# Optimization experiments

Hardware: AMD Instinct MI355X
Metric: run time of the kernel (lower is better)

The kernel has to match this reference:

```python
import jax, jax.numpy as jnp
import numpy as np

N, D, NUM_CLASSES = 4096, 1024, 1000


def setup_inputs() -> dict:
    key = jax.random.key(0)
    k1, k2 = jax.random.split(key)
    output = jax.random.normal(k1, (N, D), dtype=jnp.float32)
    target = jax.random.randint(k2, (N,), 0, NUM_CLASSES, dtype=jnp.int64)
    return {"output": output, "target": target}


def reference(output, target):
    # k1: strictly-lower-triangular part of the gram matrix [N, N]
    gram = output @ output.T
    k1 = jnp.tril(gram, -1)
    # k2: strictly-lower-triangular label-equality mask (vectorized form of
    # the original O(N^2) python double loop)
    eq = (target[:, None] == target[None, :]).astype(output.dtype)
    k2 = jnp.tril(eq, -1)
    return -(jnp.sum(k1 * k2) / (jnp.sum(k2) * jnp.linalg.norm(k1)))
```

## Files before the change

### kernel.cpp

```cpp
#include <hip/hip_runtime.h>
#include <hip/hip_bf16.h>


typedef __attribute__((ext_vector_type(8))) short short8;
typedef __attribute__((ext_vector_type(4))) float f32x4;

#define N_ROWS 4096
#define D_DIM  1024
#define N_CLS  1000
#define NTILE  32
#define NBLK   528
#define NK     32

__device__ __forceinline__ unsigned short f2bf(float f) {
  unsigned u = __float_as_uint(f);
  u += 0x7fffu + ((u >> 16) & 1u);
  return (unsigned short)(u >> 16);
}

__device__ __forceinline__ void gload16(const short* g, const char* l) {
  __builtin_amdgcn_global_load_lds(
      (const __attribute__((address_space(1))) unsigned*)g,
      (__attribute__((address_space(3))) unsigned*)(void*)l, 16, 0, 0);
}

__global__ void __launch_bounds__(256) kprep(const float* __restrict__ A,
                                             const int* __restrict__ target,
                                             short* __restrict__ Ab,
                                             double* __restrict__ rowp,
                                             double* __restrict__ cssp,
                                             int* __restrict__ cntp) {
  const int tid = threadIdx.x, lane = tid & 63, w = tid >> 6;

  if (blockIdx.x < 512) {
    __shared__ double wr2[4];
    const int row0 = blockIdx.x * 8;
    double ls = 0.0;
#pragma unroll
    for (int rr = 0; rr < 2; ++rr) {
      const int i = row0 + w * 2 + rr;
      const float4* src = (const float4*)(A + (size_t)i * D_DIM);
      short4* dst = (short4*)(Ab + (size_t)i * D_DIM);
      float s = 0.f;
#pragma unroll
      for (int c = 0; c < 4; ++c) {
        const float4 v = src[lane + c * 64];
        s += v.x * v.x + v.y * v.y + v.z * v.z + v.w * v.w;
        short4 o;
        o.x = (short)f2bf(v.x); o.y = (short)f2bf(v.y);
        o.z = (short)f2bf(v.z); o.w = (short)f2bf(v.w);
        dst[lane + c * 64] = o;
      }
#pragma unroll
      for (int off = 32; off; off >>= 1) s += __shfl_down(s, off);
      if (lane == 0) ls += (double)s;
    }
    if (lane == 0) wr2[w] = ls;
    __syncthreads();
    if (tid == 0) rowp[blockIdx.x] = wr2[0] + wr2[1] + wr2[2] + wr2[3];
  } else {
    __shared__ int list[N_ROWS];
    __shared__ int lcnt;
    __shared__ float wred[4];
    const int c = blockIdx.x - 512;
    if (c >= N_CLS) return;
    if (tid == 0) lcnt = 0;
    __syncthreads();
    for (int j = tid; j < N_ROWS; j += 256)
      if (target[j] == c) { int p = atomicAdd(&lcnt, 1); list[p] = j; }
    __syncthreads();
    const int n = lcnt;
    float4 acc = make_float4(0.f, 0.f, 0.f, 0.f);
    for (int m = 0; m < n; ++m) {
      const float4 v = *(const float4*)(A + (size_t)list[m] * D_DIM + tid * 4);
      acc.x += v.x; acc.y += v.y; acc.z += v.z; acc.w += v.w;
    }
    float s = acc.x * acc.x + acc.y * acc.y + acc.z * acc.z + acc.w * acc.w;
#pragma unroll
    for (int off = 32; off; off >>= 1) s += __shfl_down(s, off);
    if (lane == 0) wred[w] = s;
    __syncthreads();
    if (tid == 0) {
      cssp[c] = (double)(wred[0] + wred[1] + wred[2] + wred[3]);
      cntp[c] = n;
    }
  }
}

__global__ void __launch_bounds__(256, 2) kfrob(const short* __restrict__ Ab,
                                                double* __restrict__ frobp) {
  __shared__ __align__(16) short As[2][128 * 32];
  __shared__ __align__(16) short Bs[2][128 * 32];
  __shared__ double wred[4];
  const int tid = threadIdx.x, lane = tid & 63, w = tid >> 6;

  const int b = (blockIdx.x & 7) * 66 + (blockIdx.x >> 3);

  int bi = (int)((sqrtf(8.f * (float)b + 1.f) - 1.f) * 0.5f);
  while ((bi + 1) * (bi + 2) / 2 <= b) ++bi;
  while (bi * (bi + 1) / 2 > b) --bi;
  const int bj = b - bi * (bi + 1) / 2;
  const bool diag = (bi == bj);

  const short* Pa = Ab + (size_t)(bi * 128) * D_DIM;
  const short* Pb = Ab + (size_t)(bj * 128) * D_DIM;

  f32x4 acc[4][4];
#pragma unroll
  for (int m = 0; m < 4; ++m)
#pragma unroll
    for (int n = 0; n < 4; ++n) acc[m][n] = (f32x4){0.f, 0.f, 0.f, 0.f};

  const int wr = w >> 1, wc = w & 1;
  const int row16 = lane & 15, ck = lane >> 4;

  const int sr = tid >> 2;
  const int scS = (tid & 3) ^ ((sr >> 1) & 3);
  const size_t g0 = (size_t)sr * D_DIM + scS * 8;
  const size_t g1 = (size_t)(sr + 64) * D_DIM + scS * 8;
  const int l0 = w * 1024;
  const int l1 = 4096 + w * 1024;

#define STAGE(buf, k0)                                                      \
  do {                                                                      \
    gload16(Pa + g0 + (k0), (const char*)As[buf] + l0);                     \
    gload16(Pa + g1 + (k0), (const char*)As[buf] + l1);                     \
    gload16(Pb + g0 + (k0), (const char*)Bs[buf] + l0);                     \
    gload16(Pb + g1 + (k0), (const char*)Bs[buf] + l1);                     \
  } while (0)

#define SWZ(R) (((R) * 32) + ((ck ^ (((R) >> 1) & 3)) * 8))

#define COMPUTE(buf)                                                        \
  do {                                                                      \
    short8 af[4], bf[4];                                                    \
    _Pragma("unroll")                                                       \
    for (int m = 0; m < 4; ++m)                                             \
      af[m] = *(const short8*)&As[buf][SWZ(wr * 64 + m * 16 + row16)];      \
    _Pragma("unroll")                                                       \
    for (int n = 0; n < 4; ++n)                                             \
      bf[n] = *(const short8*)&Bs[buf][SWZ(wc * 64 + n * 16 + row16)];      \
    _Pragma("unroll")                                                       \
    for (int m = 0; m < 4; ++m)                                             \
      _Pragma("unroll")                                                     \
      for (int n = 0; n < 4; ++n)                                           \
        acc[m][n] = __builtin_amdgcn_mfma_f32_16x16x32_bf16(af[m], bf[n],   \
                                                            acc[m][n], 0, 0, 0);\
  } while (0)

  STAGE(0, 0);
  int cur = 0;
#pragma unroll 1
  for (int t = 0; t < NK - 1; ++t) {
    STAGE(cur ^ 1, (t + 1) * 32);
    asm volatile("s_waitcnt vmcnt(4)" ::: "memory");
    __builtin_amdgcn_sched_barrier(0);
    __builtin_amdgcn_s_barrier();
    __builtin_amdgcn_sched_barrier(0);
    COMPUTE(cur);
    asm volatile("s_waitcnt lgkmcnt(0)" ::: "memory");
    __builtin_amdgcn_sched_barrier(0);
    __builtin_amdgcn_s_barrier();
    __builtin_amdgcn_sched_barrier(0);
    cur ^= 1;
  }
  asm volatile("s_waitcnt vmcnt(0)" ::: "memory");
  __builtin_amdgcn_sched_barrier(0);
  __builtin_amdgcn_s_barrier();
  __builtin_amdgcn_sched_barrier(0);
  COMPUTE(cur);
#undef STAGE
#undef COMPUTE
#undef SWZ

  float fs = 0.f;
  if (!diag) {
#pragma unroll
    for (int m = 0; m < 4; ++m)
#pragma unroll
      for (int n = 0; n < 4; ++n)
#pragma unroll
        for (int q = 0; q < 4; ++q) fs += acc[m][n][q] * acc[m][n][q];
  } else {
    const int rbase = (lane >> 4) * 4, cbase = lane & 15;
#pragma unroll
    for (int m = 0; m < 4; ++m)
#pragma unroll
      for (int n = 0; n < 4; ++n)
#pragma unroll
        for (int q = 0; q < 4; ++q) {
          const int rl = wr * 64 + m * 16 + rbase + q;
          const int cl = wc * 64 + n * 16 + cbase;
          if (rl > cl) fs += acc[m][n][q] * acc[m][n][q];
        }
  }
#pragma unroll
  for (int off = 32; off; off >>= 1) fs += __shfl_down(fs, off);
  if (lane == 0) wred[w] = (double)fs;
  __syncthreads();
  if (tid == 0)
    frobp[b] = wred[0] + wred[1] + wred[2] + wred[3];
}

__global__ void __launch_bounds__(256) kfinal(const double* __restrict__ rowp,
                                              const double* __restrict__ cssp,
                                              const int* __restrict__ cntp,
                                              const double* __restrict__ frobp,
                                              float* __restrict__ out) {
  __shared__ double red[256];
  const int tid = threadIdx.x;
  double lsum = rowp[tid] + rowp[tid + 256];
  double lcss = 0.0, lcnn = 0.0, lfr = 0.0;
  for (int c = tid; c < N_CLS; c += 256) {
    lcss += cssp[c];
    const double nc = (double)cntp[c];
    lcnn += nc * nc;
  }
  for (int c = tid; c < NBLK; c += 256) lfr += frobp[c];

  double vals[4] = {lsum, lcss, lcnn, lfr};
  double res[4];
  for (int v = 0; v < 4; ++v) {
    red[tid] = vals[v];
    __syncthreads();
    for (int s = 128; s; s >>= 1) {
      if (tid < s) red[tid] += red[tid + s];
      __syncthreads();
    }
    res[v] = red[0];
    __syncthreads();
  }
  if (tid == 0) {
    const double sumr = res[0], css = res[1], cnn = res[2], frob = res[3];
    const double S1 = 0.5 * (css - sumr);
    const double S2 = 0.5 * (cnn - (double)N_ROWS);
    const double S3 = frob;
    out[0] = (float)(-(S1 / (S2 * sqrt(S3))));
  }
}

extern "C" void kernel_launch(void* const* d_in, const int* in_sizes, int n_in,
                              void* d_out, int out_size, void* d_ws, size_t ws_size,
                              hipStream_t stream) {
  const float* A = (const float*)d_in[0];
  const int* target = (const int*)d_in[1];
  float* out = (float*)d_out;

  char* ws = (char*)d_ws;
  short*  Ab    = (short*)ws;
  double* rowp  = (double*)(ws + 8388608);
  double* cssp  = (double*)(ws + 8388608 + 4096);
  int*    cntp  = (int*)   (ws + 8388608 + 4096 + 8000);
  double* frobp = (double*)(ws + 8388608 + 4096 + 8000 + 4096);

  kprep<<<512 + N_CLS, 256, 0, stream>>>(A, target, Ab, rowp, cssp, cntp);
  kfrob<<<NBLK, 256, 0, stream>>>(Ab, frobp);
  kfinal<<<1, 256, 0, stream>>>(rowp, cssp, cntp, frobp, out);
}
```

Before: 46.96 us.

## Compute Frobenius norm via small D×D Gram matrix A^T A with split-K

Uses the identity ||AA^T||_F^2 = ||A^T A||_F^2, so the Gram is computed on the 1024x1024 A^T A (symmetric lower tiles) instead of the 4096x4096 output. The prep kernel now transposes A to bf16 and stores per-row squared norms; the strict-lower sum is recovered as half of (total minus the sum of squared row norms). The GEMM is split across 8 K-chunks writing partial tiles to a slab, with a new reduction kernel summing them. This cuts matmul work roughly fourfold but adds a transpose, a large slab write/read and an extra launch. Subtracting the diagonal term may also cost precision.

```diff
diff --git a/kernel.cpp b/kernel.cpp
--- a/kernel.cpp
+++ b/kernel.cpp
@@ -8,9 +8,9 @@
 #define N_ROWS 4096
 #define D_DIM  1024
 #define N_CLS  1000
-#define NTILE  32
-#define NBLK   528
-#define NK     32
+#define NCHUNK 8
+#define NTIL   36
+#define NKG    16
 
 __device__ __forceinline__ unsigned short f2bf(float f) {
   unsigned u = __float_as_uint(f);
@@ -26,43 +26,46 @@
 
 __global__ void __launch_bounds__(256) kprep(const float* __restrict__ A,
                                              const int* __restrict__ target,
-                                             short* __restrict__ Ab,
-                                             double* __restrict__ rowp,
+                                             short* __restrict__ At,
+                                             float* __restrict__ rowsqp,
                                              double* __restrict__ cssp,
                                              int* __restrict__ cntp) {
   const int tid = threadIdx.x, lane = tid & 63, w = tid >> 6;
 
-  if (blockIdx.x < 512) {
-    __shared__ double wr2[4];
-    const int row0 = blockIdx.x * 8;
-    double ls = 0.0;
-#pragma unroll
-    for (int rr = 0; rr < 2; ++rr) {
-      const int i = row0 + w * 2 + rr;
-      const float4* src = (const float4*)(A + (size_t)i * D_DIM);
-      short4* dst = (short4*)(Ab + (size_t)i * D_DIM);
-      float s = 0.f;
-#pragma unroll
-      for (int c = 0; c < 4; ++c) {
-        const float4 v = src[lane + c * 64];
-        s += v.x * v.x + v.y * v.y + v.z * v.z + v.w * v.w;
-        short4 o;
-        o.x = (short)f2bf(v.x); o.y = (short)f2bf(v.y);
-        o.z = (short)f2bf(v.z); o.w = (short)f2bf(v.w);
-        dst[lane + c * 64] = o;
-      }
-#pragma unroll
-      for (int off = 32; off; off >>= 1) s += __shfl_down(s, off);
-      if (lane == 0) ls += (double)s;
-    }
-    if (lane == 0) wr2[w] = ls;
-    __syncthreads();
-    if (tid == 0) rowp[blockIdx.x] = wr2[0] + wr2[1] + wr2[2] + wr2[3];
+  if (blockIdx.x < 1024) {
+    __shared__ short tile[64 * 68];
+    const int bx = blockIdx.x & 63, by = blockIdx.x >> 6;
+    const int i0 = bx * 64, d0 = by * 64;
+    const int c16 = tid & 15, rgrp = tid >> 4;
+#pragma unroll
+    for (int rr = 0; rr < 4; ++rr) {
+      const int row = rgrp + rr * 16;
+      const float4 v = *(const float4*)(A + (size_t)(i0 + row) * D_DIM + d0 + c16 * 4);
+      tile[(c16 * 4 + 0) * 68 + row] = (short)f2bf(v.x);
+      tile[(c16 * 4 + 1) * 68 + row] = (short)f2bf(v.y);
+      tile[(c16 * 4 + 2) * 68 + row] = (short)f2bf(v.z);
+      tile[(c16 * 4 + 3) * 68 + row] = (short)f2bf(v.w);
+      float s = v.x * v.x + v.y * v.y + v.z * v.z + v.w * v.w;
+#pragma unroll
+      for (int off = 1; off < 16; off <<= 1) s += __shfl_xor(s, off);
+      if (c16 == 0) rowsqp[(by << 12) + i0 + row] = s;
+    }
+    __syncthreads();
+    const int wrow = tid >> 2, wc = tid & 3;
+    short8 s0, s1;
+#pragma unroll
+    for (int q = 0; q < 8; ++q) {
+      s0[q] = tile[wrow * 68 + wc * 16 + q];
+      s1[q] = tile[wrow * 68 + wc * 16 + 8 + q];
+    }
+    short* dst = At + (size_t)(d0 + wrow) * N_ROWS + i0 + wc * 16;
+    *(short8*)(dst)     = s0;
+    *(short8*)(dst + 8) = s1;
   } else {
     __shared__ int list[N_ROWS];
     __shared__ int lcnt;
     __shared__ float wred[4];
-    const int c = blockIdx.x - 512;
+    const int c = blockIdx.x - 1024;
     if (c >= N_CLS) return;
     if (tid == 0) lcnt = 0;
     __syncthreads();
@@ -87,23 +90,22 @@
   }
 }
 
-__global__ void __launch_bounds__(256, 2) kfrob(const short* __restrict__ Ab,
-                                                double* __restrict__ frobp) {
+__global__ void __launch_bounds__(256, 2) kgemm(const short* __restrict__ At,
+                                                float* __restrict__ slab) {
   __shared__ __align__(16) short As[2][128 * 32];
   __shared__ __align__(16) short Bs[2][128 * 32];
-  __shared__ double wred[4];
   const int tid = threadIdx.x, lane = tid & 63, w = tid >> 6;
 
-  const int b = (blockIdx.x & 7) * 66 + (blockIdx.x >> 3);
-
-  int bi = (int)((sqrtf(8.f * (float)b + 1.f) - 1.f) * 0.5f);
-  while ((bi + 1) * (bi + 2) / 2 <= b) ++bi;
-  while (bi * (bi + 1) / 2 > b) --bi;
-  const int bj = b - bi * (bi + 1) / 2;
-  const bool diag = (bi == bj);
-
-  const short* Pa = Ab + (size_t)(bi * 128) * D_DIM;
-  const short* Pb = Ab + (size_t)(bj * 128) * D_DIM;
+  const int c  = blockIdx.x & 7;
+  const int tt = blockIdx.x >> 3;
+
+  int bi = (int)((sqrtf(8.f * (float)tt + 1.f) - 1.f) * 0.5f);
+  while ((bi + 1) * (bi + 2) / 2 <= tt) ++bi;
+  while (bi * (bi + 1) / 2 > tt) --bi;
+  const int bj = tt - bi * (bi + 1) / 2;
+
+  const short* Pa = At + (size_t)(bi * 128) * N_ROWS + c * 512;
+  const short* Pb = At + (size_t)(bj * 128) * N_ROWS + c * 512;
 
   f32x4 acc[4][4];
 #pragma unroll
@@ -116,8 +118,8 @@
 
   const int sr = tid >> 2;
   const int scS = (tid & 3) ^ ((sr >> 1) & 3);
-  const size_t g0 = (size_t)sr * D_DIM + scS * 8;
-  const size_t g1 = (size_t)(sr + 64) * D_DIM + scS * 8;
+  const size_t g0 = (size_t)sr * N_ROWS + scS * 8;
+  const size_t g1 = (size_t)(sr + 64) * N_ROWS + scS * 8;
   const int l0 = w * 1024;
   const int l1 = 4096 + w * 1024;
 
@@ -151,7 +153,7 @@
   STAGE(0, 0);
   int cur = 0;
 #pragma unroll 1
-  for (int t = 0; t < NK - 1; ++t) {
+  for (int t = 0; t < NKG - 1; ++t) {
     STAGE(cur ^ 1, (t + 1) * 32);
     asm volatile("s_waitcnt vmcnt(4)" ::: "memory");
     __builtin_amdgcn_sched_barrier(0);
@@ -173,54 +175,83 @@
 #undef COMPUTE
 #undef SWZ
 
+  f32x4* sp = (f32x4*)slab + ((size_t)(c * NTIL + tt) * 16) * 256 + tid;
+#pragma unroll
+  for (int m = 0; m < 4; ++m)
+#pragma unroll
+    for (int n = 0; n < 4; ++n)
+      sp[(size_t)(m * 4 + n) * 256] = acc[m][n];
+}
+
+__global__ void __launch_bounds__(256) kred(const float* __restrict__ slab,
+                                            double* __restrict__ frobp2) {
+  __shared__ double wred[4];
+  const int tid = threadIdx.x, lane = tid & 63, w = tid >> 6;
+  const int tt = blockIdx.x;
+
+  int bi = (int)((sqrtf(8.f * (float)tt + 1.f) - 1.f) * 0.5f);
+  while ((bi + 1) * (bi + 2) / 2 <= tt) ++bi;
+  while (bi * (bi + 1) / 2 > tt) --bi;
+  const int bj = tt - bi * (bi + 1) / 2;
+  const bool diag = (bi == bj);
+
+  const int wr = w >> 1, wc = w & 1;
+  const int rbase = (lane >> 4) * 4, cbase = lane & 15;
+  const f32x4* sb = (const f32x4*)slab;
+
   float fs = 0.f;
-  if (!diag) {
-#pragma unroll
-    for (int m = 0; m < 4; ++m)
-#pragma unroll
-      for (int n = 0; n < 4; ++n)
-#pragma unroll
-        for (int q = 0; q < 4; ++q) fs += acc[m][n][q] * acc[m][n][q];
-  } else {
-    const int rbase = (lane >> 4) * 4, cbase = lane & 15;
-#pragma unroll
-    for (int m = 0; m < 4; ++m)
-#pragma unroll
-      for (int n = 0; n < 4; ++n)
-#pragma unroll
-        for (int q = 0; q < 4; ++q) {
-          const int rl = wr * 64 + m * 16 + rbase + q;
-          const int cl = wc * 64 + n * 16 + cbase;
-          if (rl > cl) fs += acc[m][n][q] * acc[m][n][q];
-        }
+#pragma unroll
+  for (int f = 0; f < 16; ++f) {
+    f32x4 v = (f32x4){0.f, 0.f, 0.f, 0.f};
+#pragma unroll
+    for (int c = 0; c < NCHUNK; ++c)
+      v += sb[((size_t)(c * NTIL + tt) * 16 + f) * 256 + tid];
+    const int m = f >> 2, n = f & 3;
+    if (!diag) {
+      fs += 2.f * (v[0] * v[0] + v[1] * v[1] + v[2] * v[2] + v[3] * v[3]);
+    } else {
+      const int cl = wc * 64 + n * 16 + cbase;
+#pragma unroll
+      for (int q = 0; q < 4; ++q) {
+        const int rl = wr * 64 + m * 16 + rbase + q;
+        const float wgt = (rl > cl) ? 2.f : ((rl == cl) ? 1.f : 0.f);
+        fs += wgt * v[q] * v[q];
+      }
+    }
   }
 #pragma unroll
   for (int off = 32; off; off >>= 1) fs += __shfl_down(fs, off);
   if (lane == 0) wred[w] = (double)fs;
   __syncthreads();
   if (tid == 0)
-    frobp[b] = wred[0] + wred[1] + wred[2] + wred[3];
-}
-
-__global__ void __launch_bounds__(256) kfinal(const double* __restrict__ rowp,
+    frobp2[tt] = wred[0] + wred[1] + wred[2] + wred[3];
+}
+
+__global__ void __launch_bounds__(256) kfinal(const float* __restrict__ rowsqp,
                                               const double* __restrict__ cssp,
                                               const int* __restrict__ cntp,
-                                              const double* __restrict__ frobp,
+                                              const double* __restrict__ frobp2,
                                               float* __restrict__ out) {
   __shared__ double red[256];
   const int tid = threadIdx.x;
-  double lsum = rowp[tid] + rowp[tid + 256];
-  double lcss = 0.0, lcnn = 0.0, lfr = 0.0;
+  double lsum = 0.0, lsq = 0.0, lcss = 0.0, lcnn = 0.0, lfr = 0.0;
+  for (int i = tid; i < N_ROWS; i += 256) {
+    float r = 0.f;
+#pragma unroll
+    for (int b = 0; b < 16; ++b) r += rowsqp[(b << 12) + i];
+    lsum += (double)r;
+    lsq  += (double)r * (double)r;
+  }
   for (int c = tid; c < N_CLS; c += 256) {
     lcss += cssp[c];
     const double nc = (double)cntp[c];
     lcnn += nc * nc;
   }
-  for (int c = tid; c < NBLK; c += 256) lfr += frobp[c];
-
-  double vals[4] = {lsum, lcss, lcnn, lfr};
-  double res[4];
-  for (int v = 0; v < 4; ++v) {
+  if (tid < NTIL) lfr = frobp2[tid];
+
+  double vals[5] = {lsum, lsq, lcss, lcnn, lfr};
+  double res[5];
+  for (int v = 0; v < 5; ++v) {
     red[tid] = vals[v];
     __syncthreads();
     for (int s = 128; s; s >>= 1) {
@@ -231,10 +262,10 @@
     __syncthreads();
   }
   if (tid == 0) {
-    const double sumr = res[0], css = res[1], cnn = res[2], frob = res[3];
+    const double sumr = res[0], sumq = res[1], css = res[2], cnn = res[3], F = res[4];
     const double S1 = 0.5 * (css - sumr);
     const double S2 = 0.5 * (cnn - (double)N_ROWS);
-    const double S3 = frob;
+    const double S3 = 0.5 * (F - sumq);
     out[0] = (float)(-(S1 / (S2 * sqrt(S3))));
   }
 }
@@ -247,13 +278,15 @@
   float* out = (float*)d_out;
 
   char* ws = (char*)d_ws;
-  short*  Ab    = (short*)ws;
-  double* rowp  = (double*)(ws + 8388608);
-  double* cssp  = (double*)(ws + 8388608 + 4096);
-  int*    cntp  = (int*)   (ws + 8388608 + 4096 + 8000);
-  double* frobp = (double*)(ws + 8388608 + 4096 + 8000 + 4096);
-
-  kprep<<<512 + N_CLS, 256, 0, stream>>>(A, target, Ab, rowp, cssp, cntp);
-  kfrob<<<NBLK, 256, 0, stream>>>(Ab, frobp);
-  kfinal<<<1, 256, 0, stream>>>(rowp, cssp, cntp, frobp, out);
-}
+  short*  At     = (short*)ws;
+  float*  slab   = (float*)(ws + 8388608);
+  float*  rowsqp = (float*)(ws + 27262976);
+  double* cssp   = (double*)(ws + 27525120);
+  int*    cntp   = (int*)   (ws + 27533312);
+  double* frobp2 = (double*)(ws + 27537408);
+
+  kprep<<<1024 + N_CLS, 256, 0, stream>>>(A, target, At, rowsqp, cssp, cntp);
+  kgemm<<<NCHUNK * NTIL, 256, 0, stream>>>(At, slab);
+  kred<<<NTIL, 256, 0, stream>>>(slab, frobp2);
+  kfinal<<<1, 256, 0, stream>>>(rowsqp, cssp, cntp, frobp2, out);
+}
```

Measured after the change: 59.72 us. 27.2% more time.

## Enlarge Gram tiles to 256x256 and co-schedule class sums with GEMM

Applied to the files above, without the earlier changes.

Gram-matrix tiles grow from 128x128 to 256x256 with 512-thread blocks, so there are 136 tiles instead of 528. Each block does more work per staged k-slice, which means fewer reloads of Ab from global memory. The per-class sum computation moves out of the conversion kernel and into the same launch as the GEMM tiles, so that work fills the many idle CUs. The risks are only 136 heavy tiles on a large GPU, which can give poor load balance, and higher register pressure from 32 accumulators per thread.

```diff
diff --git a/kernel.cpp b/kernel.cpp
--- a/kernel.cpp
+++ b/kernel.cpp
@@ -8,8 +8,7 @@
 #define N_ROWS 4096
 #define D_DIM  1024
 #define N_CLS  1000
-#define NTILE  32
-#define NBLK   528
+#define NTIL   136
 #define NK     32
 
 __device__ __forceinline__ unsigned short f2bf(float f) {
@@ -24,182 +23,193 @@
       (__attribute__((address_space(3))) unsigned*)(void*)l, 16, 0, 0);
 }
 
-__global__ void __launch_bounds__(256) kprep(const float* __restrict__ A,
-                                             const int* __restrict__ target,
+__global__ void __launch_bounds__(256) kconv(const float* __restrict__ A,
                                              short* __restrict__ Ab,
-                                             double* __restrict__ rowp,
-                                             double* __restrict__ cssp,
-                                             int* __restrict__ cntp) {
+                                             double* __restrict__ rowp) {
+  __shared__ double wr2[4];
   const int tid = threadIdx.x, lane = tid & 63, w = tid >> 6;
-
-  if (blockIdx.x < 512) {
-    __shared__ double wr2[4];
-    const int row0 = blockIdx.x * 8;
-    double ls = 0.0;
-#pragma unroll
-    for (int rr = 0; rr < 2; ++rr) {
-      const int i = row0 + w * 2 + rr;
-      const float4* src = (const float4*)(A + (size_t)i * D_DIM);
-      short4* dst = (short4*)(Ab + (size_t)i * D_DIM);
-      float s = 0.f;
-#pragma unroll
-      for (int c = 0; c < 4; ++c) {
-        const float4 v = src[lane + c * 64];
-        s += v.x * v.x + v.y * v.y + v.z * v.z + v.w * v.w;
-        short4 o;
-        o.x = (short)f2bf(v.x); o.y = (short)f2bf(v.y);
-        o.z = (short)f2bf(v.z); o.w = (short)f2bf(v.w);
-        dst[lane + c * 64] = o;
-      }
-#pragma unroll
-      for (int off = 32; off; off >>= 1) s += __shfl_down(s, off);
-      if (lane == 0) ls += (double)s;
-    }
-    if (lane == 0) wr2[w] = ls;
-    __syncthreads();
-    if (tid == 0) rowp[blockIdx.x] = wr2[0] + wr2[1] + wr2[2] + wr2[3];
-  } else {
-    __shared__ int list[N_ROWS];
-    __shared__ int lcnt;
-    __shared__ float wred[4];
-    const int c = blockIdx.x - 512;
-    if (c >= N_CLS) return;
-    if (tid == 0) lcnt = 0;
-    __syncthreads();
-    for (int j = tid; j < N_ROWS; j += 256)
-      if (target[j] == c) { int p = atomicAdd(&lcnt, 1); list[p] = j; }
-    __syncthreads();
-    const int n = lcnt;
-    float4 acc = make_float4(0.f, 0.f, 0.f, 0.f);
-    for (int m = 0; m < n; ++m) {
-      const float4 v = *(const float4*)(A + (size_t)list[m] * D_DIM + tid * 4);
-      acc.x += v.x; acc.y += v.y; acc.z += v.z; acc.w += v.w;
-    }
-    float s = acc.x * acc.x + acc.y * acc.y + acc.z * acc.z + acc.w * acc.w;
+  const int row0 = blockIdx.x * 8;
+  double ls = 0.0;
+#pragma unroll
+  for (int rr = 0; rr < 2; ++rr) {
+    const int i = row0 + w * 2 + rr;
+    const float4* src = (const float4*)(A + (size_t)i * D_DIM);
+    short4* dst = (short4*)(Ab + (size_t)i * D_DIM);
+    float s = 0.f;
+#pragma unroll
+    for (int c = 0; c < 4; ++c) {
+      const float4 v = src[lane + c * 64];
+      s += v.x * v.x + v.y * v.y + v.z * v.z + v.w * v.w;
+      short4 o;
+      o.x = (short)f2bf(v.x); o.y = (short)f2bf(v.y);
+      o.z = (short)f2bf(v.z); o.w = (short)f2bf(v.w);
+      dst[lane + c * 64] = o;
+    }
 #pragma unroll
     for (int off = 32; off; off >>= 1) s += __shfl_down(s, off);
-    if (lane == 0) wred[w] = s;
-    __syncthreads();
-    if (tid == 0) {
-      cssp[c] = (double)(wred[0] + wred[1] + wred[2] + wred[3]);
-      cntp[c] = n;
-    }
-  }
-}
-
-__global__ void __launch_bounds__(256, 2) kfrob(const short* __restrict__ Ab,
-                                                double* __restrict__ frobp) {
-  __shared__ __align__(16) short As[2][128 * 32];
-  __shared__ __align__(16) short Bs[2][128 * 32];
-  __shared__ double wred[4];
+    if (lane == 0) ls += (double)s;
+  }
+  if (lane == 0) wr2[w] = ls;
+  __syncthreads();
+  if (tid == 0) rowp[blockIdx.x] = wr2[0] + wr2[1] + wr2[2] + wr2[3];
+}
+
+__global__ void __launch_bounds__(512, 2) kmain(const float* __restrict__ A,
+                                                const int* __restrict__ target,
+                                                const short* __restrict__ Ab,
+                                                double* __restrict__ frobp,
+                                                double* __restrict__ cssp,
+                                                int* __restrict__ cntp) {
+  __shared__ __align__(16) char smem[65600];
   const int tid = threadIdx.x, lane = tid & 63, w = tid >> 6;
 
-  const int b = (blockIdx.x & 7) * 66 + (blockIdx.x >> 3);
-
-  int bi = (int)((sqrtf(8.f * (float)b + 1.f) - 1.f) * 0.5f);
-  while ((bi + 1) * (bi + 2) / 2 <= b) ++bi;
-  while (bi * (bi + 1) / 2 > b) --bi;
-  const int bj = b - bi * (bi + 1) / 2;
-  const bool diag = (bi == bj);
-
-  const short* Pa = Ab + (size_t)(bi * 128) * D_DIM;
-  const short* Pb = Ab + (size_t)(bj * 128) * D_DIM;
-
-  f32x4 acc[4][4];
-#pragma unroll
-  for (int m = 0; m < 4; ++m)
-#pragma unroll
-    for (int n = 0; n < 4; ++n) acc[m][n] = (f32x4){0.f, 0.f, 0.f, 0.f};
-
-  const int wr = w >> 1, wc = w & 1;
-  const int row16 = lane & 15, ck = lane >> 4;
-
-  const int sr = tid >> 2;
-  const int scS = (tid & 3) ^ ((sr >> 1) & 3);
-  const size_t g0 = (size_t)sr * D_DIM + scS * 8;
-  const size_t g1 = (size_t)(sr + 64) * D_DIM + scS * 8;
-  const int l0 = w * 1024;
-  const int l1 = 4096 + w * 1024;
+  if (blockIdx.x < NTIL) {
+    double* wredd = (double*)(smem + 65536);
+
+    const int b = (blockIdx.x & 7) * 17 + (blockIdx.x >> 3);
+    int bi = (int)((sqrtf(8.f * (float)b + 1.f) - 1.f) * 0.5f);
+    while ((bi + 1) * (bi + 2) / 2 <= b) ++bi;
+    while (bi * (bi + 1) / 2 > b) --bi;
+    const int bj = b - bi * (bi + 1) / 2;
+    const bool diag = (bi == bj);
+
+    const short* Pa = Ab + (size_t)(bi * 256) * D_DIM;
+    const short* Pb = Ab + (size_t)(bj * 256) * D_DIM;
+
+    f32x4 acc[8][4];
+#pragma unroll
+    for (int m = 0; m < 8; ++m)
+#pragma unroll
+      for (int n = 0; n < 4; ++n) acc[m][n] = (f32x4){0.f, 0.f, 0.f, 0.f};
+
+    const int wr = w >> 2, wc = w & 3;
+    const int row16 = lane & 15, ck = lane >> 4;
+
+    const int sr = tid >> 2;
+    const int scS = (tid & 3) ^ ((sr >> 1) & 3);
+    const size_t g0 = (size_t)sr * D_DIM + scS * 8;
+    const size_t g1 = (size_t)(sr + 128) * D_DIM + scS * 8;
+    const int l0 = w * 1024;
+    const int l1 = 8192 + w * 1024;
+
+#define ASB(buf) (smem + (buf) * 16384)
+#define BSB(buf) (smem + 32768 + (buf) * 16384)
 
 #define STAGE(buf, k0)                                                      \
-  do {                                                                      \
-    gload16(Pa + g0 + (k0), (const char*)As[buf] + l0);                     \
-    gload16(Pa + g1 + (k0), (const char*)As[buf] + l1);                     \
-    gload16(Pb + g0 + (k0), (const char*)Bs[buf] + l0);                     \
-    gload16(Pb + g1 + (k0), (const char*)Bs[buf] + l1);                     \
-  } while (0)
+    do {                                                                    \
+      gload16(Pa + g0 + (k0), ASB(buf) + l0);                               \
+      gload16(Pa + g1 + (k0), ASB(buf) + l1);                               \
+      gload16(Pb + g0 + (k0), BSB(buf) + l0);                               \
+      gload16(Pb + g1 + (k0), BSB(buf) + l1);                               \
+    } while (0)
 
 #define SWZ(R) (((R) * 32) + ((ck ^ (((R) >> 1) & 3)) * 8))
 
 #define COMPUTE(buf)                                                        \
-  do {                                                                      \
-    short8 af[4], bf[4];                                                    \
-    _Pragma("unroll")                                                       \
-    for (int m = 0; m < 4; ++m)                                             \
-      af[m] = *(const short8*)&As[buf][SWZ(wr * 64 + m * 16 + row16)];      \
-    _Pragma("unroll")                                                       \
-    for (int n = 0; n < 4; ++n)                                             \
-      bf[n] = *(const short8*)&Bs[buf][SWZ(wc * 64 + n * 16 + row16)];      \
-    _Pragma("unroll")                                                       \
-    for (int m = 0; m < 4; ++m)                                             \
+    do {                                                                    \
+      short8 af[8], bf[4];                                                  \
+      _Pragma("unroll")                                                     \
+      for (int m = 0; m < 8; ++m)                                           \
+        af[m] = *(const short8*)((short*)ASB(buf) + SWZ(wr * 128 + m * 16 + row16)); \
       _Pragma("unroll")                                                     \
       for (int n = 0; n < 4; ++n)                                           \
-        acc[m][n] = __builtin_amdgcn_mfma_f32_16x16x32_bf16(af[m], bf[n],   \
-                                                            acc[m][n], 0, 0, 0);\
-  } while (0)
-
-  STAGE(0, 0);
-  int cur = 0;
+        bf[n] = *(const short8*)((short*)BSB(buf) + SWZ(wc * 64 + n * 16 + row16)); \
+      _Pragma("unroll")                                                     \
+      for (int m = 0; m < 8; ++m)                                           \
+        _Pragma("unroll")                                                   \
+        for (int n = 0; n < 4; ++n)                                         \
+          acc[m][n] = __builtin_amdgcn_mfma_f32_16x16x32_bf16(af[m], bf[n], \
+                                                              acc[m][n], 0, 0, 0); \
+    } while (0)
+
+    STAGE(0, 0);
+    int cur = 0;
 #pragma unroll 1
-  for (int t = 0; t < NK - 1; ++t) {
-    STAGE(cur ^ 1, (t + 1) * 32);
-    asm volatile("s_waitcnt vmcnt(4)" ::: "memory");
+    for (int t = 0; t < NK - 1; ++t) {
+      STAGE(cur ^ 1, (t + 1) * 32);
+      asm volatile("s_waitcnt vmcnt(4)" ::: "memory");
+      __builtin_amdgcn_sched_barrier(0);
+      __builtin_amdgcn_s_barrier();
+      __builtin_amdgcn_sched_barrier(0);
+      COMPUTE(cur);
+      asm volatile("s_waitcnt lgkmcnt(0)" ::: "memory");
+      __builtin_amdgcn_sched_barrier(0);
+      __builtin_amdgcn_s_barrier();
+      __builtin_amdgcn_sched_barrier(0);
+      cur ^= 1;
+    }
+    asm volatile("s_waitcnt vmcnt(0)" ::: "memory");
     __builtin_amdgcn_sched_barrier(0);
     __builtin_amdgcn_s_barrier();
     __builtin_amdgcn_sched_barrier(0);
     COMPUTE(cur);
-    asm volatile("s_waitcnt lgkmcnt(0)" ::: "memory");
-    __builtin_amdgcn_sched_barrier(0);
-    __builtin_amdgcn_s_barrier();
-    __builtin_amdgcn_sched_barrier(0);
-    cur ^= 1;
-  }
-  asm volatile("s_waitcnt vmcnt(0)" ::: "memory");
-  __builtin_amdgcn_sched_barrier(0);
-  __builtin_amdgcn_s_barrier();
-  __builtin_amdgcn_sched_barrier(0);
-  COMPUTE(cur);
 #undef STAGE
 #undef COMPUTE
 #undef SWZ
-
-  float fs = 0.f;
-  if (!diag) {
-#pragma unroll
-    for (int m = 0; m < 4; ++m)
-#pragma unroll
-      for (int n = 0; n < 4; ++n)
-#pragma unroll
-        for (int q = 0; q < 4; ++q) fs += acc[m][n][q] * acc[m][n][q];
+#undef ASB
+#undef BSB
+
+    float fs = 0.f;
+    if (!diag) {
+#pragma unroll
+      for (int m = 0; m < 8; ++m)
+#pragma unroll
+        for (int n = 0; n < 4; ++n)
+#pragma unroll
+          for (int q = 0; q < 4; ++q) fs += acc[m][n][q] * acc[m][n][q];
+    } else {
+      const int rbase = (lane >> 4) * 4, cbase = lane & 15;
+#pragma unroll
+      for (int m = 0; m < 8; ++m)
+#pragma unroll
+        for (int n = 0; n < 4; ++n)
+#pragma unroll
+          for (int q = 0; q < 4; ++q) {
+            const int rl = wr * 128 + m * 16 + rbase + q;
+            const int cl = wc * 64 + n * 16 + cbase;
+            if (rl > cl) fs += acc[m][n][q] * acc[m][n][q];
+          }
+    }
+#pragma unroll
+    for (int off = 32; off; off >>= 1) fs += __shfl_down(fs, off);
+    if (lane == 0) wredd[w] = (double)fs;
+    __syncthreads();
+    if (tid == 0) {
+      double t = 0.0;
+#pragma unroll
+      for (int i = 0; i < 8; ++i) t += wredd[i];
+      frobp[b] = t;
+    }
   } else {
-    const int rbase = (lane >> 4) * 4, cbase = lane & 15;
-#pragma unroll
-    for (int m = 0; m < 4; ++m)
-#pragma unroll
-      for (int n = 0; n < 4; ++n)
-#pragma unroll
-        for (int q = 0; q < 4; ++q) {
-          const int rl = wr * 64 + m * 16 + rbase + q;
-          const int cl = wc * 64 + n * 16 + cbase;
-          if (rl > cl) fs += acc[m][n][q] * acc[m][n][q];
-        }
-  }
-#pragma unroll
-  for (int off = 32; off; off >>= 1) fs += __shfl_down(fs, off);
-  if (lane == 0) wred[w] = (double)fs;
-  __syncthreads();
-  if (tid == 0)
-    frobp[b] = wred[0] + wred[1] + wred[2] + wred[3];
+    int* list = (int*)smem;
+    int* lcnt = (int*)(smem + 16384);
+    float* wredf = (float*)(smem + 16400);
+    const int c = blockIdx.x - NTIL;
+    if (c >= N_CLS) return;
+    if (tid == 0) *lcnt = 0;
+    __syncthreads();
+    for (int j = tid; j < N_ROWS; j += 512)
+      if (target[j] == c) { int p = atomicAdd(lcnt, 1); list[p] = j; }
+    __syncthreads();
+    const int n = *lcnt;
+    float2 acc = make_float2(0.f, 0.f);
+    for (int m = 0; m < n; ++m) {
+      const float2 v = *(const float2*)(A + (size_t)list[m] * D_DIM + tid * 2);
+      acc.x += v.x; acc.y += v.y;
+    }
+    float s = acc.x * acc.x + acc.y * acc.y;
+#pragma unroll
+    for (int off = 32; off; off >>= 1) s += __shfl_down(s, off);
+    if (lane == 0) wredf[w] = s;
+    __syncthreads();
+    if (tid == 0) {
+      float t = 0.f;
+#pragma unroll
+      for (int i = 0; i < 8; ++i) t += wredf[i];
+      cssp[c] = (double)t;
+      cntp[c] = n;
+    }
+  }
 }
 
 __global__ void __launch_bounds__(256) kfinal(const double* __restrict__ rowp,
@@ -216,7 +226,7 @@
     const double nc = (double)cntp[c];
     lcnn += nc * nc;
   }
-  for (int c = tid; c < NBLK; c += 256) lfr += frobp[c];
+  if (tid < NTIL) lfr = frobp[tid];
 
   double vals[4] = {lsum, lcss, lcnn, lfr};
   double res[4];
@@ -253,7 +263,7 @@
   int*    cntp  = (int*)   (ws + 8388608 + 4096 + 8000);
   double* frobp = (double*)(ws + 8388608 + 4096 + 8000 + 4096);
 
-  kprep<<<512 + N_CLS, 256, 0, stream>>>(A, target, Ab, rowp, cssp, cntp);
-  kfrob<<<NBLK, 256, 0, stream>>>(Ab, frobp);
+  kconv<<<512, 256, 0, stream>>>(A, Ab, rowp);
+  kmain<<<NTIL + N_CLS, 512, 0, stream>>>(A, target, Ab, frobp, cssp, cntp);
   kfinal<<<1, 256, 0, stream>>>(rowp, cssp, cntp, frobp, out);
 }
```

New measurement: 46.95 us. Within noise of the previous version (-0.0%).
